# Kernel tuning notes

Measured on AMD Instinct MI355X. Metric: run time of the kernel, lower is better.

The kernel has to match this reference:

```python
import jax, jax.numpy as jnp
import numpy as np

VOCAB = 512
T = 64
D = 32
N_NODES = 4000
N_LAYERS = 5
EDGE_P = 0.03
N_BIAS = 2
SEED = 0
BATCH = 512
N_IN = T * D  # 2048 input nodes (flattened [T, d_model])


def build_graph():
    """Deterministic layered random-wired DAG.

    Node layout: [0, N_IN) inputs | [N_IN, N_IN+N_BIAS) bias(=1) |
    hidden layers | last VOCAB nodes = outputs (logits).
    An edge (u -> v) exists with prob EDGE_P for any u in an earlier
    layer than v; every non-input node gets >=1 incoming edge.
    Returns (layers, total_edges) where each layer entry is
    (src_ids, dst_local, layer_start, layer_size, w_lo, w_hi).
    """
    rng = np.random.RandomState(SEED)
    n_hidden = N_NODES - (N_IN + N_BIAS) - VOCAB
    sizes = [n_hidden // N_LAYERS + (1 if i < n_hidden % N_LAYERS else 0)
             for i in range(N_LAYERS)] + [VOCAB]
    layers = []
    start = N_IN + N_BIAS  # nodes with ids < start are valid sources
    offset = 0
    for size in sizes:
        mask = rng.random((start, size)) < EDGE_P
        empty = np.where(mask.sum(axis=0) == 0)[0]
        if empty.size:
            mask[rng.randint(0, start, empty.size), empty] = True
        src, dst = np.nonzero(mask)
        n_e = src.size
        layers.append((src.astype(np.int32), dst.astype(np.int32),
                       start, size, offset, offset + n_e))
        offset += n_e
        start += size
    return layers, offset


def setup_inputs() -> dict:
    key = jax.random.key(0)
    k1, k2, k3, k4 = jax.random.split(key, 4)
    _, n_edges = build_graph()
    return {
        "ids": jax.random.randint(k1, (BATCH, T), 0, VOCAB),
        "token_emb": jax.random.normal(k2, (VOCAB, D), dtype=jnp.float32) * 0.02,
        "pos_emb": jax.random.normal(k3, (T, D), dtype=jnp.float32) * 0.02,
        "weights": jax.random.normal(k4, (n_edges,), dtype=jnp.float32) * 0.05,
    }


def reference(ids, token_emb, pos_emb, weights):
    layers, _ = build_graph()  # static (numpy, trace-time)
    B = ids.shape[0]
    # embedding lookup + positional add, flatten to the RWNN input slab
    emb = token_emb[ids] + pos_emb[None, :, :]          # [B, T, D]
    flat = emb.reshape(B, N_IN)                          # [B, n_in]
    vals = jnp.concatenate(
        [flat, jnp.ones((B, N_BIAS), flat.dtype)], axis=1)  # [B, n_in+n_bias]
    n_layers_total = len(layers)
    for li, (src, dst, start, size, w0, w1) in enumerate(layers):
        # irregular gather over all predecessor nodes, scale, scatter-add
        msg = vals[:, src] * weights[w0:w1]              # [B, E_l]
        pre = jnp.zeros((B, size), flat.dtype).at[:, dst].add(msg)
        h = pre if li == n_layers_total - 1 else jnp.tanh(pre)
        vals = jnp.concatenate([vals, h], axis=1)
    return vals[:, -VOCAB:]                              # logits [B, V]
```

## Files before the change

### kernel.cpp

```cpp
#include <hip/hip_runtime.h>
#include <cstdint>
#include <cstdlib>
#include <cstring>
#include <vector>

#define RW_VOCAB 512
#define RW_T 64
#define RW_D 32
#define RW_NIN 2048
#define RW_NBIAS 2
#define RW_BATCH 512
#define RW_NLAYERS 6
#define RW_VBLD 4096

typedef __attribute__((ext_vector_type(8))) short short8;
typedef __attribute__((ext_vector_type(4))) float f32x4;

namespace {

struct MT19937 {
  uint32_t mt[624];
  int mti;
  void seed(uint32_t s) {
    for (int i = 0; i < 624; ++i) {
      mt[i] = s;
      s = 1812433253u * (s ^ (s >> 30)) + (uint32_t)i + 1u;
    }
    mti = 624;
  }
  inline uint32_t next() {
    if (mti >= 624) {
      for (int i = 0; i < 624; ++i) {
        uint32_t y = (mt[i] & 0x80000000u) | (mt[(i + 1) % 624] & 0x7fffffffu);
        mt[i] = mt[(i + 397) % 624] ^ (y >> 1) ^ ((y & 1u) ? 2567483615u : 0u);
      }
      mti = 0;
    }
    uint32_t y = mt[mti++];
    y ^= y >> 11;
    y ^= (y << 7) & 2636928640u;
    y ^= (y << 15) & 4022730752u;
    y ^= y >> 18;
    return y;
  }
  inline double rnd() {
    uint32_t a = next() >> 5, b = next() >> 6;
    return ((double)a * 67108864.0 + (double)b) / 9007199254740992.0;
  }
};

const int LAYER_SIZES[RW_NLAYERS] = {288, 288, 288, 287, 287, 512};
const int LAYER_START[RW_NLAYERS] = {2050, 2338, 2626, 2914, 3201, 3488};
const int LAYER_NPAD[RW_NLAYERS]  = {288, 288, 288, 288, 288, 512};
const int LAYER_NT[RW_NLAYERS]    = {9, 9, 9, 9, 9, 16};

struct GArgsH {
  int p0[RW_NLAYERS], ep[RW_NLAYERS], er[RW_NLAYERS], w0[RW_NLAYERS];
  int kpad[RW_NLAYERS];
  unsigned wofs[RW_NLAYERS];
};

struct HostGraph {
  int Epad;
  GArgsH ga;
  unsigned wdt_elems;
  uint32_t* h_pack;
};

HostGraph* build_host_graph() {
  auto* G = new HostGraph();
  MT19937 mt;
  mt.seed(0);
  std::vector<uint32_t> pack;
  pack.reserve(180000);
  int start = RW_NIN + RW_NBIAS;
  int wcum = 0;
  for (int li = 0; li < RW_NLAYERS; ++li) {
    const int size = LAYER_SIZES[li];
    G->ga.p0[li] = (int)pack.size();
    G->ga.w0[li] = wcum;
    int cnt = 0;
    for (int u = 0; u < start; ++u) {
      for (int v = 0; v < size; ++v) {
        if (mt.rnd() < 0.03) {
          pack.push_back(((uint32_t)v << 12) | (uint32_t)u);
          ++cnt;
        }
      }
    }
    G->ga.er[li] = cnt;
    wcum += cnt;
    while (pack.size() & 3u) pack.push_back(0u);
    G->ga.ep[li] = (int)pack.size() - G->ga.p0[li];
    start += size;
  }
  G->Epad = (int)pack.size();
  unsigned ofs = 0;
  for (int li = 0; li < RW_NLAYERS; ++li) {
    G->ga.kpad[li] = ((LAYER_START[li] + 63) / 64) * 64;
    G->ga.wofs[li] = ofs;
    ofs += (unsigned)LAYER_NPAD[li] * (unsigned)G->ga.kpad[li];
  }
  G->wdt_elems = ofs;
  const size_t bytes = (size_t)G->Epad * 4;
  if (hipHostMalloc((void**)&G->h_pack, bytes) != hipSuccess)
    G->h_pack = (uint32_t*)malloc(bytes);
  memcpy(G->h_pack, pack.data(), bytes);
  return G;
}

}

struct GArgs {
  int p0[RW_NLAYERS], ep[RW_NLAYERS], er[RW_NLAYERS], w0[RW_NLAYERS];
  int kpad[RW_NLAYERS];
  unsigned wofs[RW_NLAYERS];
};

__device__ __forceinline__ unsigned short f2bf(float f) {
  unsigned u = __builtin_bit_cast(unsigned, f);
  return (unsigned short)((u + 0x7fffu + ((u >> 16) & 1u)) >> 16);
}

__global__ __launch_bounds__(256) void rwnn_init(
    unsigned* __restrict__ wdt32, int nwdt32, float* __restrict__ pre,
    unsigned* __restrict__ vb32, const int* __restrict__ ids,
    const float* __restrict__ tok, const float* __restrict__ pos) {
  const int gt = blockIdx.x * 256 + threadIdx.x;
  const int gs = gridDim.x * 256;
  for (int i = gt; i < nwdt32; i += gs) wdt32[i] = 0u;
  for (int i = gt; i < RW_BATCH * 512; i += gs) pre[i] = 0.0f;
  for (int i = gt; i < RW_BATCH * (RW_VBLD / 2); i += gs) {
    const int b = i >> 11, j = i & 2047;
    const int c0 = j * 2;
    unsigned dw;
    if (c0 >= RW_NIN + RW_NBIAS) {
      dw = 0u;
    } else if (c0 == RW_NIN) {
      dw = 0x3f803f80u;
    } else {
      const int t = c0 >> 5, d = c0 & 31;
      const int id = ids[b * RW_T + t];
      const float v0 = tok[id * 32 + d] + pos[c0];
      const float v1 = tok[id * 32 + d + 1] + pos[c0 + 1];
      dw = (unsigned)f2bf(v0) | ((unsigned)f2bf(v1) << 16);
    }
    vb32[i] = dw;
  }
}

__global__ __launch_bounds__(256) void rwnn_scatter(
    const uint32_t* __restrict__ pack, const float* __restrict__ w,
    unsigned short* __restrict__ wdt, GArgs ga, int Epad) {
  const int i = blockIdx.x * 256 + threadIdx.x;
  if (i >= Epad) return;
  int l = 0;
#pragma unroll
  for (int k = 1; k < RW_NLAYERS; ++k)
    if (i >= ga.p0[k]) l = k;
  const int kk = i - ga.p0[l];
  if (kk >= ga.er[l]) return;
  const uint32_t pk = pack[i];
  const unsigned u = pk & 4095u, v = pk >> 12;
  wdt[ga.wofs[l] + (size_t)v * (unsigned)ga.kpad[l] + u] = f2bf(w[ga.w0[l] + kk]);
}

__global__ __launch_bounds__(256) void rwnn_gemm(
    const unsigned short* __restrict__ Vb, const unsigned short* __restrict__ Bt,
    float* __restrict__ pre, int kpad, int ck) {
  __shared__ unsigned short As[128][32];
  __shared__ unsigned short Bs[32][32];
  const int tid = threadIdx.x;
  const int wave = tid >> 6, lane = tid & 63;
  const int mtile = blockIdx.x, ntile = blockIdx.y;
  const int k0 = blockIdx.z * ck;
  const int k1 = min(k0 + ck, kpad);
  if (k0 >= k1) return;
  f32x4 acc[2][2] = {};
  const int sr = tid >> 2, sc = (tid & 3) * 8;
  for (int k = k0; k < k1; k += 32) {
    __syncthreads();
    {
      const float4 v0 =
          *(const float4*)(Vb + (size_t)(mtile * 128 + sr) * RW_VBLD + k + sc);
      *(float4*)(&As[sr][sc]) = v0;
      const float4 v1 = *(const float4*)(Vb +
          (size_t)(mtile * 128 + sr + 64) * RW_VBLD + k + sc);
      *(float4*)(&As[sr + 64][sc]) = v1;
    }
    if (tid < 128) {
      *(float4*)(&Bs[sr][sc]) =
          *(const float4*)(Bt + (size_t)(ntile * 32 + sr) * kpad + k + sc);
    }
    __syncthreads();
    const int lr = lane & 15, lk = (lane >> 4) * 8;
    const short8 a0 = *(const short8*)(&As[wave * 32 + lr][lk]);
    const short8 a1 = *(const short8*)(&As[wave * 32 + 16 + lr][lk]);
    const short8 b0 = *(const short8*)(&Bs[lr][lk]);
    const short8 b1 = *(const short8*)(&Bs[16 + lr][lk]);
    acc[0][0] = __builtin_amdgcn_mfma_f32_16x16x32_bf16(a0, b0, acc[0][0], 0, 0, 0);
    acc[0][1] = __builtin_amdgcn_mfma_f32_16x16x32_bf16(a0, b1, acc[0][1], 0, 0, 0);
    acc[1][0] = __builtin_amdgcn_mfma_f32_16x16x32_bf16(a1, b0, acc[1][0], 0, 0, 0);
    acc[1][1] = __builtin_amdgcn_mfma_f32_16x16x32_bf16(a1, b1, acc[1][1], 0, 0, 0);
  }
  const int lr = lane & 15, lq = lane >> 4;
#pragma unroll
  for (int ms = 0; ms < 2; ++ms)
#pragma unroll
    for (int ns = 0; ns < 2; ++ns)
#pragma unroll
      for (int r = 0; r < 4; ++r) {
        const int grow = mtile * 128 + wave * 32 + ms * 16 + lq * 4 + r;
        const int gcol = ntile * 32 + ns * 16 + lr;
        atomicAdd(pre + (size_t)grow * 512 + gcol, acc[ms][ns][r]);
      }
}

__global__ __launch_bounds__(256) void rwnn_epi(
    float* __restrict__ pre, unsigned short* __restrict__ Vb,
    float* __restrict__ out, int start, int nsize, int last) {
  const int b = blockIdx.x;
  for (int n = threadIdx.x; n < 512; n += 256) {
    const float v = pre[(size_t)b * 512 + n];
    pre[(size_t)b * 512 + n] = 0.0f;
    if (n < nsize) {
      if (last)
        out[(size_t)b * 512 + n] = v;
      else
        Vb[(size_t)b * RW_VBLD + start + n] = f2bf(tanhf(v));
    }
  }
}

__global__ __launch_bounds__(256) void rwnn_build_w(const float* __restrict__ w,
                                                    float* __restrict__ wpad,
                                                    GArgs ga, int Epad) {
  const int i = blockIdx.x * 256 + threadIdx.x;
  if (i >= Epad) return;
  int l = 0;
#pragma unroll
  for (int k = 1; k < RW_NLAYERS; ++k)
    if (i >= ga.p0[k]) l = k;
  const int kk = i - ga.p0[l];
  wpad[i] = (kk < ga.er[l]) ? w[ga.w0[l] + kk] : 0.0f;
}

__global__ __launch_bounds__(512) void rwnn_fwd_sparse(
    const int* __restrict__ ids, const float* __restrict__ tok,
    const float* __restrict__ pos, const uint32_t* __restrict__ pack,
    const float* __restrict__ wpad, float* __restrict__ out, GArgs ga) {
  __shared__ float vals[4000];
  const int b = blockIdx.x;
  const int tid = threadIdx.x;
  for (int i = tid; i < RW_NIN; i += 512) {
    const int t = i >> 5, d = i & 31;
    vals[i] = tok[(ids[b * RW_T + t] << 5) + d] + pos[i];
  }
  if (tid < RW_NBIAS) vals[RW_NIN + tid] = 1.0f;
  const int sizes[RW_NLAYERS] = {288, 288, 288, 287, 287, 512};
  int nb = RW_NIN + RW_NBIAS;
  for (int li = 0; li < RW_NLAYERS; ++li) {
    const int size = sizes[li];
    __syncthreads();
    for (int v = tid; v < size; v += 512) vals[nb + v] = 0.0f;
    __syncthreads();
    const int p0 = ga.p0[li], ng = ga.ep[li] >> 2;
    for (int g = tid; g < ng; g += 512) {
      const int e = p0 + (g << 2);
      const uint4 pk = *reinterpret_cast<const uint4*>(pack + e);
      const float4 wv = *reinterpret_cast<const float4*>(wpad + e);
      atomicAdd(&vals[nb + (pk.x >> 12)], vals[pk.x & 4095u] * wv.x);
      atomicAdd(&vals[nb + (pk.y >> 12)], vals[pk.y & 4095u] * wv.y);
      atomicAdd(&vals[nb + (pk.z >> 12)], vals[pk.z & 4095u] * wv.z);
      atomicAdd(&vals[nb + (pk.w >> 12)], vals[pk.w & 4095u] * wv.w);
    }
    __syncthreads();
    if (li == RW_NLAYERS - 1) {
      for (int v = tid; v < RW_VOCAB; v += 512) out[b * RW_VOCAB + v] = vals[nb + v];
    } else {
      for (int v = tid; v < size; v += 512) vals[nb + v] = tanhf(vals[nb + v]);
    }
    nb += size;
  }
}

extern "C" void kernel_launch(void* const* d_in, const int* in_sizes, int n_in,
                              void* d_out, int out_size, void* d_ws,
                              size_t ws_size, hipStream_t stream) {
  static HostGraph* G = build_host_graph();
  const int Epad = G->Epad;

  const int* ids = (const int*)d_in[0];
  const float* tok = (const float*)d_in[1];
  const float* pos = (const float*)d_in[2];
  const float* w = (const float*)d_in[3];
  float* out = (float*)d_out;

  GArgs ga;
  memcpy(&ga, &G->ga, sizeof(GArgs));

  char* ws = (char*)d_ws;
  const size_t packB = ((size_t)Epad * 4 + 255) & ~(size_t)255;
  const size_t wdtB = ((size_t)G->wdt_elems * 2 + 255) & ~(size_t)255;
  const size_t vbB = (size_t)RW_BATCH * RW_VBLD * 2;
  const size_t preB = (size_t)RW_BATCH * 512 * 4;
  const size_t need = packB + wdtB + vbB + preB;

  uint32_t* d_pack = (uint32_t*)ws;
  hipMemcpyAsync(d_pack, G->h_pack, (size_t)Epad * 4, hipMemcpyHostToDevice,
                 stream);

  if (ws_size < need) {
    float* d_wpad = (float*)(ws + packB);
    rwnn_build_w<<<(Epad + 255) / 256, 256, 0, stream>>>(w, d_wpad, ga, Epad);
    rwnn_fwd_sparse<<<RW_BATCH, 512, 0, stream>>>(ids, tok, pos, d_pack, d_wpad,
                                                  out, ga);
    return;
  }

  unsigned short* d_wdt = (unsigned short*)(ws + packB);
  unsigned short* d_vb = (unsigned short*)(ws + packB + wdtB);
  float* d_pre = (float*)(ws + packB + wdtB + vbB);

  rwnn_init<<<2048, 256, 0, stream>>>((unsigned*)d_wdt,
                                      (int)(G->wdt_elems / 2), d_pre,
                                      (unsigned*)d_vb, ids, tok, pos);
  rwnn_scatter<<<(Epad + 255) / 256, 256, 0, stream>>>(d_pack, w, d_wdt, ga,
                                                       Epad);
  for (int l = 0; l < RW_NLAYERS; ++l) {
    const int nt = LAYER_NT[l];
    const int SK = (l == RW_NLAYERS - 1) ? 4 : 7;
    const int kpad = ga.kpad[l];
    const int ck = (((kpad + SK - 1) / SK) + 31) & ~31;
    rwnn_gemm<<<dim3(4, nt, SK), 256, 0, stream>>>(
        d_vb, d_wdt + ga.wofs[l], d_pre, kpad, ck);
    rwnn_epi<<<RW_BATCH, 256, 0, stream>>>(d_pre, d_vb, out, LAYER_START[l],
                                           LAYER_SIZES[l],
                                           l == RW_NLAYERS - 1 ? 1 : 0);
  }
}
```

Measured before the change: 171.3 us.

## Fuse split-K reduction and tanh epilogue into GEMM via slabs and counters

The GEMM no longer atomically adds into a shared pre-activation buffer followed by a separate epilogue kernel. Each split-K block writes its partial tile to its own slab, and the last block to arrive, tracked by a per-tile atomic counter, sums the slabs and applies tanh or writes the logits. It also adds double-buffered LDS staging through global_load_lds with an XOR swizzle, and vectorizes the init kernel. This removes six epilogue launches, the float atomics and the zeroing of the pre buffer, at the cost of extra slab memory traffic and threadfence synchronization.

```diff
diff --git a/kernel.cpp b/kernel.cpp
--- a/kernel.cpp
+++ b/kernel.cpp
@@ -6,15 +6,16 @@
 
 #define RW_VOCAB 512
 #define RW_T 64
-#define RW_D 32
 #define RW_NIN 2048
 #define RW_NBIAS 2
 #define RW_BATCH 512
 #define RW_NLAYERS 6
 #define RW_VBLD 4096
+#define SLABSTRIDE (512 * 512)
 
 typedef __attribute__((ext_vector_type(8))) short short8;
 typedef __attribute__((ext_vector_type(4))) float f32x4;
+typedef uint32_t u32;
 
 namespace {
 
@@ -51,8 +52,9 @@
 
 const int LAYER_SIZES[RW_NLAYERS] = {288, 288, 288, 287, 287, 512};
 const int LAYER_START[RW_NLAYERS] = {2050, 2338, 2626, 2914, 3201, 3488};
-const int LAYER_NPAD[RW_NLAYERS]  = {288, 288, 288, 288, 288, 512};
-const int LAYER_NT[RW_NLAYERS]    = {9, 9, 9, 9, 9, 16};
+const int LAYER_NPAD[RW_NLAYERS] = {288, 288, 288, 288, 288, 512};
+const int LAYER_NT[RW_NLAYERS] = {9, 9, 9, 9, 9, 16};
+const int LAYER_SK[RW_NLAYERS] = {7, 7, 7, 7, 7, 4};
 
 struct GArgsH {
   int p0[RW_NLAYERS], ep[RW_NLAYERS], er[RW_NLAYERS], w0[RW_NLAYERS];
@@ -122,31 +124,40 @@
   return (unsigned short)((u + 0x7fffu + ((u >> 16) & 1u)) >> 16);
 }
 
+__device__ __forceinline__ void gll16(const void* g, void* l) {
+  __builtin_amdgcn_global_load_lds(
+      (const __attribute__((address_space(1))) u32*)g,
+      (__attribute__((address_space(3))) u32*)l, 16, 0, 0);
+}
+
 __global__ __launch_bounds__(256) void rwnn_init(
-    unsigned* __restrict__ wdt32, int nwdt32, float* __restrict__ pre,
-    unsigned* __restrict__ vb32, const int* __restrict__ ids,
-    const float* __restrict__ tok, const float* __restrict__ pos) {
+    uint4* __restrict__ wdt4, int n4, uint4* __restrict__ vb4,
+    const int* __restrict__ ids, const float* __restrict__ tok,
+    const float* __restrict__ pos, int* __restrict__ cnt) {
   const int gt = blockIdx.x * 256 + threadIdx.x;
   const int gs = gridDim.x * 256;
-  for (int i = gt; i < nwdt32; i += gs) wdt32[i] = 0u;
-  for (int i = gt; i < RW_BATCH * 512; i += gs) pre[i] = 0.0f;
-  for (int i = gt; i < RW_BATCH * (RW_VBLD / 2); i += gs) {
-    const int b = i >> 11, j = i & 2047;
-    const int c0 = j * 2;
-    unsigned dw;
-    if (c0 >= RW_NIN + RW_NBIAS) {
-      dw = 0u;
+  const uint4 z = {0u, 0u, 0u, 0u};
+  for (int i = gt; i < n4; i += gs) wdt4[i] = z;
+  for (int i = gt; i < RW_BATCH * (RW_VBLD / 8); i += gs) {
+    const int b = i >> 9, j = i & 511;
+    const int c0 = j * 8;
+    uint4 val = z;
+    if (c0 + 8 <= RW_NIN) {
+      const int id = ids[b * RW_T + (c0 >> 5)];
+      const float4 t0 = *(const float4*)(tok + id * 32 + (c0 & 31));
+      const float4 t1 = *(const float4*)(tok + id * 32 + (c0 & 31) + 4);
+      const float4 p0 = *(const float4*)(pos + c0);
+      const float4 p1 = *(const float4*)(pos + c0 + 4);
+      val.x = (u32)f2bf(t0.x + p0.x) | ((u32)f2bf(t0.y + p0.y) << 16);
+      val.y = (u32)f2bf(t0.z + p0.z) | ((u32)f2bf(t0.w + p0.w) << 16);
+      val.z = (u32)f2bf(t1.x + p1.x) | ((u32)f2bf(t1.y + p1.y) << 16);
+      val.w = (u32)f2bf(t1.z + p1.z) | ((u32)f2bf(t1.w + p1.w) << 16);
     } else if (c0 == RW_NIN) {
-      dw = 0x3f803f80u;
-    } else {
-      const int t = c0 >> 5, d = c0 & 31;
-      const int id = ids[b * RW_T + t];
-      const float v0 = tok[id * 32 + d] + pos[c0];
-      const float v1 = tok[id * 32 + d + 1] + pos[c0 + 1];
-      dw = (unsigned)f2bf(v0) | ((unsigned)f2bf(v1) << 16);
-    }
-    vb32[i] = dw;
-  }
+      val.x = 0x3f803f80u;
+    }
+    vb4[(size_t)b * (RW_VBLD / 8) + j] = val;
+  }
+  if (gt < RW_NLAYERS * 64) cnt[gt] = 0;
 }
 
 __global__ __launch_bounds__(256) void rwnn_scatter(
@@ -162,72 +173,112 @@
   if (kk >= ga.er[l]) return;
   const uint32_t pk = pack[i];
   const unsigned u = pk & 4095u, v = pk >> 12;
-  wdt[ga.wofs[l] + (size_t)v * (unsigned)ga.kpad[l] + u] = f2bf(w[ga.w0[l] + kk]);
-}
+  wdt[ga.wofs[l] + (size_t)v * (unsigned)ga.kpad[l] + u] =
+      f2bf(w[ga.w0[l] + kk]);
+}
+
+struct GemmP {
+  int kpad, ck, SK, nsize, vstart, last, cntofs;
+  unsigned wofs;
+};
 
 __global__ __launch_bounds__(256) void rwnn_gemm(
-    const unsigned short* __restrict__ Vb, const unsigned short* __restrict__ Bt,
-    float* __restrict__ pre, int kpad, int ck) {
-  __shared__ unsigned short As[128][32];
-  __shared__ unsigned short Bs[32][32];
+    const unsigned short* __restrict__ Vb,
+    const unsigned short* __restrict__ wdt, float* __restrict__ slab,
+    int* __restrict__ cnt, unsigned short* __restrict__ VbW,
+    float* __restrict__ out, GemmP P) {
+  __shared__ unsigned short As[2][128 * 32];
+  __shared__ unsigned short Bs[2][32 * 32];
+  __shared__ int fin;
+  const unsigned short* Bt = wdt + P.wofs;
   const int tid = threadIdx.x;
   const int wave = tid >> 6, lane = tid & 63;
-  const int mtile = blockIdx.x, ntile = blockIdx.y;
-  const int k0 = blockIdx.z * ck;
-  const int k1 = min(k0 + ck, kpad);
-  if (k0 >= k1) return;
+  const int mt = blockIdx.x, nt = blockIdx.y, sk = blockIdx.z;
+  const int k0 = sk * P.ck;
+  const int k1 = min(k0 + P.ck, P.kpad);
+  const int nit = (k1 > k0) ? ((k1 - k0 + 31) >> 5) : 0;
+
+  const int srow = tid >> 2;
+  const int schunk = tid & 3;
+
   f32x4 acc[2][2] = {};
-  const int sr = tid >> 2, sc = (tid & 3) * 8;
-  for (int k = k0; k < k1; k += 32) {
-    __syncthreads();
-    {
-      const float4 v0 =
-          *(const float4*)(Vb + (size_t)(mtile * 128 + sr) * RW_VBLD + k + sc);
-      *(float4*)(&As[sr][sc]) = v0;
-      const float4 v1 = *(const float4*)(Vb +
-          (size_t)(mtile * 128 + sr + 64) * RW_VBLD + k + sc);
-      *(float4*)(&As[sr + 64][sc]) = v1;
-    }
-    if (tid < 128) {
-      *(float4*)(&Bs[sr][sc]) =
-          *(const float4*)(Bt + (size_t)(ntile * 32 + sr) * kpad + k + sc);
-    }
-    __syncthreads();
-    const int lr = lane & 15, lk = (lane >> 4) * 8;
-    const short8 a0 = *(const short8*)(&As[wave * 32 + lr][lk]);
-    const short8 a1 = *(const short8*)(&As[wave * 32 + 16 + lr][lk]);
-    const short8 b0 = *(const short8*)(&Bs[lr][lk]);
-    const short8 b1 = *(const short8*)(&Bs[16 + lr][lk]);
+
+#define STAGE(bf, kk)                                                        \
+  do {                                                                       \
+    _Pragma("unroll") for (int j = 0; j < 2; ++j) {                          \
+      const int row_ = j * 64 + srow;                                        \
+      const int gc_ = schunk ^ (row_ & 3);                                   \
+      gll16(Vb + (size_t)(mt * 128 + row_) * RW_VBLD + (kk) + gc_ * 8,       \
+            (char*)(&As[bf][0]) + j * 4096 + wave * 1024);                   \
+    }                                                                        \
+    if (wave < 2) {                                                          \
+      const int gc_ = schunk ^ (srow & 3);                                   \
+      gll16(Bt + (size_t)(nt * 32 + srow) * P.kpad + (kk) + gc_ * 8,         \
+            (char*)(&Bs[bf][0]) + wave * 1024);                              \
+    }                                                                        \
+  } while (0)
+
+  if (nit > 0) STAGE(0, k0);
+  __syncthreads();
+
+  const int lr = lane & 15, gc4 = lane >> 4;
+  const int ra0 = wave * 32 + lr;
+  const int oa0 = ra0 * 64 + ((gc4 ^ (ra0 & 3)) << 4);
+  const int oa1 = oa0 + 16 * 64;
+  const int ob0 = lr * 64 + ((gc4 ^ (lr & 3)) << 4);
+  const int ob1 = ob0 + 16 * 64;
+
+  for (int t = 0; t < nit; ++t) {
+    const int bf = t & 1;
+    if (t + 1 < nit) STAGE(bf ^ 1, k0 + (t + 1) * 32);
+    const char* a = (const char*)&As[bf][0];
+    const char* bb = (const char*)&Bs[bf][0];
+    const short8 a0 = *(const short8*)(a + oa0);
+    const short8 a1 = *(const short8*)(a + oa1);
+    const short8 b0 = *(const short8*)(bb + ob0);
+    const short8 b1 = *(const short8*)(bb + ob1);
     acc[0][0] = __builtin_amdgcn_mfma_f32_16x16x32_bf16(a0, b0, acc[0][0], 0, 0, 0);
     acc[0][1] = __builtin_amdgcn_mfma_f32_16x16x32_bf16(a0, b1, acc[0][1], 0, 0, 0);
     acc[1][0] = __builtin_amdgcn_mfma_f32_16x16x32_bf16(a1, b0, acc[1][0], 0, 0, 0);
     acc[1][1] = __builtin_amdgcn_mfma_f32_16x16x32_bf16(a1, b1, acc[1][1], 0, 0, 0);
-  }
-  const int lr = lane & 15, lq = lane >> 4;
-#pragma unroll
-  for (int ms = 0; ms < 2; ++ms)
-#pragma unroll
-    for (int ns = 0; ns < 2; ++ns)
-#pragma unroll
-      for (int r = 0; r < 4; ++r) {
-        const int grow = mtile * 128 + wave * 32 + ms * 16 + lq * 4 + r;
-        const int gcol = ntile * 32 + ns * 16 + lr;
-        atomicAdd(pre + (size_t)grow * 512 + gcol, acc[ms][ns][r]);
-      }
-}
-
-__global__ __launch_bounds__(256) void rwnn_epi(
-    float* __restrict__ pre, unsigned short* __restrict__ Vb,
-    float* __restrict__ out, int start, int nsize, int last) {
-  const int b = blockIdx.x;
-  for (int n = threadIdx.x; n < 512; n += 256) {
-    const float v = pre[(size_t)b * 512 + n];
-    pre[(size_t)b * 512 + n] = 0.0f;
-    if (n < nsize) {
-      if (last)
-        out[(size_t)b * 512 + n] = v;
-      else
-        Vb[(size_t)b * RW_VBLD + start + n] = f2bf(tanhf(v));
+    __syncthreads();
+  }
+#undef STAGE
+
+  {
+    float* sl = slab + (size_t)sk * SLABSTRIDE;
+    const int lq = lane >> 4;
+#pragma unroll
+    for (int ms = 0; ms < 2; ++ms)
+#pragma unroll
+      for (int ns = 0; ns < 2; ++ns)
+#pragma unroll
+        for (int r = 0; r < 4; ++r) {
+          const int grow = mt * 128 + wave * 32 + ms * 16 + lq * 4 + r;
+          const int gcol = nt * 32 + ns * 16 + lr;
+          sl[(size_t)grow * 512 + gcol] = acc[ms][ns][r];
+        }
+  }
+  __syncthreads();
+  if (tid == 0) {
+    __threadfence();
+    fin = (atomicAdd(cnt + P.cntofs + mt * 16 + nt, 1) == P.SK - 1) ? 1 : 0;
+  }
+  __syncthreads();
+  if (fin) {
+    __threadfence();
+    const int c = tid & 31;
+    const int gcol = nt * 32 + c;
+    const bool wr = P.last ? true : (gcol < P.nsize);
+    for (int rr = tid >> 5; rr < 128; rr += 8) {
+      const int grow = mt * 128 + rr;
+      float s = 0.f;
+      for (int q = 0; q < P.SK; ++q)
+        s += slab[(size_t)q * SLABSTRIDE + (size_t)grow * 512 + gcol];
+      if (P.last)
+        out[(size_t)grow * 512 + gcol] = s;
+      else if (wr)
+        VbW[(size_t)grow * RW_VBLD + P.vstart + gcol] = f2bf(tanhf(s));
     }
   }
 }
@@ -276,7 +327,8 @@
     }
     __syncthreads();
     if (li == RW_NLAYERS - 1) {
-      for (int v = tid; v < RW_VOCAB; v += 512) out[b * RW_VOCAB + v] = vals[nb + v];
+      for (int v = tid; v < RW_VOCAB; v += 512)
+        out[b * RW_VOCAB + v] = vals[nb + v];
     } else {
       for (int v = tid; v < size; v += 512) vals[nb + v] = tanhf(vals[nb + v]);
     }
@@ -303,8 +355,9 @@
   const size_t packB = ((size_t)Epad * 4 + 255) & ~(size_t)255;
   const size_t wdtB = ((size_t)G->wdt_elems * 2 + 255) & ~(size_t)255;
   const size_t vbB = (size_t)RW_BATCH * RW_VBLD * 2;
-  const size_t preB = (size_t)RW_BATCH * 512 * 4;
-  const size_t need = packB + wdtB + vbB + preB;
+  const size_t slabB = (size_t)7 * SLABSTRIDE * 4;
+  const size_t cntB = RW_NLAYERS * 64 * 4;
+  const size_t need = packB + wdtB + vbB + slabB + cntB;
 
   uint32_t* d_pack = (uint32_t*)ws;
   hipMemcpyAsync(d_pack, G->h_pack, (size_t)Epad * 4, hipMemcpyHostToDevice,
@@ -313,29 +366,31 @@
   if (ws_size < need) {
     float* d_wpad = (float*)(ws + packB);
     rwnn_build_w<<<(Epad + 255) / 256, 256, 0, stream>>>(w, d_wpad, ga, Epad);
-    rwnn_fwd_sparse<<<RW_BATCH, 512, 0, stream>>>(ids, tok, pos, d_pack, d_wpad,
-                                                  out, ga);
+    rwnn_fwd_sparse<<<RW_BATCH, 512, 0, stream>>>(ids, tok, pos, d_pack,
+                                                  d_wpad, out, ga);
     return;
   }
 
   unsigned short* d_wdt = (unsigned short*)(ws + packB);
   unsigned short* d_vb = (unsigned short*)(ws + packB + wdtB);
-  float* d_pre = (float*)(ws + packB + wdtB + vbB);
-
-  rwnn_init<<<2048, 256, 0, stream>>>((unsigned*)d_wdt,
-                                      (int)(G->wdt_elems / 2), d_pre,
-                                      (unsigned*)d_vb, ids, tok, pos);
+  float* d_slab = (float*)(ws + packB + wdtB + vbB);
+  int* d_cnt = (int*)(ws + packB + wdtB + vbB + slabB);
+
+  rwnn_init<<<1024, 256, 0, stream>>>((uint4*)d_wdt, (int)(G->wdt_elems / 8),
+                                      (uint4*)d_vb, ids, tok, pos, d_cnt);
   rwnn_scatter<<<(Epad + 255) / 256, 256, 0, stream>>>(d_pack, w, d_wdt, ga,
                                                        Epad);
   for (int l = 0; l < RW_NLAYERS; ++l) {
-    const int nt = LAYER_NT[l];
-    const int SK = (l == RW_NLAYERS - 1) ? 4 : 7;
-    const int kpad = ga.kpad[l];
-    const int ck = (((kpad + SK - 1) / SK) + 31) & ~31;
-    rwnn_gemm<<<dim3(4, nt, SK), 256, 0, stream>>>(
-        d_vb, d_wdt + ga.wofs[l], d_pre, kpad, ck);
-    rwnn_epi<<<RW_BATCH, 256, 0, stream>>>(d_pre, d_vb, out, LAYER_START[l],
-                                           LAYER_SIZES[l],
-                                           l == RW_NLAYERS - 1 ? 1 : 0);
-  }
-}
+    GemmP P;
+    P.kpad = ga.kpad[l];
+    P.SK = LAYER_SK[l];
+    P.ck = ((P.kpad + P.SK - 1) / P.SK + 31) & ~31;
+    P.nsize = LAYER_SIZES[l];
+    P.vstart = LAYER_START[l];
+    P.last = (l == RW_NLAYERS - 1) ? 1 : 0;
+    P.cntofs = l * 64;
+    P.wofs = ga.wofs[l];
+    rwnn_gemm<<<dim3(4, LAYER_NT[l], P.SK), 256, 0, stream>>>(
+        d_vb, d_wdt, d_slab, d_cnt, d_vb, out, P);
+  }
+}
```

Result: slower. 382.4 us (+123.3%).

## Double K tile, swizzle LDS and prefetch next tile into registers in GEMM

Applied to the files above, without the earlier changes.

The bf16 MFMA GEMM now stages a 64-wide K slice per iteration instead of 32. It stores tiles into shared memory with an XOR swizzle to avoid bank conflicts, and loads the next K slice from global memory into registers while the current slice is being multiplied. The init kernel is also vectorised to 16-byte stores and float4 embedding loads, and launches half as many blocks. The split-K chunk is rounded to 64, so reads can run past the true K end unless kpad is padded with zeros. The early return for empty splits is also removed.

```diff
diff --git a/kernel.cpp b/kernel.cpp
--- a/kernel.cpp
+++ b/kernel.cpp
@@ -6,7 +6,6 @@
 
 #define RW_VOCAB 512
 #define RW_T 64
-#define RW_D 32
 #define RW_NIN 2048
 #define RW_NBIAS 2
 #define RW_BATCH 512
@@ -15,6 +14,7 @@
 
 typedef __attribute__((ext_vector_type(8))) short short8;
 typedef __attribute__((ext_vector_type(4))) float f32x4;
+typedef uint32_t u32;
 
 namespace {
 
@@ -51,8 +51,9 @@
 
 const int LAYER_SIZES[RW_NLAYERS] = {288, 288, 288, 287, 287, 512};
 const int LAYER_START[RW_NLAYERS] = {2050, 2338, 2626, 2914, 3201, 3488};
-const int LAYER_NPAD[RW_NLAYERS]  = {288, 288, 288, 288, 288, 512};
-const int LAYER_NT[RW_NLAYERS]    = {9, 9, 9, 9, 9, 16};
+const int LAYER_NPAD[RW_NLAYERS] = {288, 288, 288, 288, 288, 512};
+const int LAYER_NT[RW_NLAYERS] = {9, 9, 9, 9, 9, 16};
+const int LAYER_SK[RW_NLAYERS] = {7, 7, 7, 7, 7, 4};
 
 struct GArgsH {
   int p0[RW_NLAYERS], ep[RW_NLAYERS], er[RW_NLAYERS], w0[RW_NLAYERS];
@@ -123,29 +124,32 @@
 }
 
 __global__ __launch_bounds__(256) void rwnn_init(
-    unsigned* __restrict__ wdt32, int nwdt32, float* __restrict__ pre,
-    unsigned* __restrict__ vb32, const int* __restrict__ ids,
+    uint4* __restrict__ wdt4, int n4, uint4* __restrict__ pre4,
+    uint4* __restrict__ vb4, const int* __restrict__ ids,
     const float* __restrict__ tok, const float* __restrict__ pos) {
   const int gt = blockIdx.x * 256 + threadIdx.x;
   const int gs = gridDim.x * 256;
-  for (int i = gt; i < nwdt32; i += gs) wdt32[i] = 0u;
-  for (int i = gt; i < RW_BATCH * 512; i += gs) pre[i] = 0.0f;
-  for (int i = gt; i < RW_BATCH * (RW_VBLD / 2); i += gs) {
-    const int b = i >> 11, j = i & 2047;
-    const int c0 = j * 2;
-    unsigned dw;
-    if (c0 >= RW_NIN + RW_NBIAS) {
-      dw = 0u;
+  const uint4 z = {0u, 0u, 0u, 0u};
+  for (int i = gt; i < n4; i += gs) wdt4[i] = z;
+  for (int i = gt; i < RW_BATCH * 512 / 4; i += gs) pre4[i] = z;
+  for (int i = gt; i < RW_BATCH * (RW_VBLD / 8); i += gs) {
+    const int b = i >> 9, j = i & 511;
+    const int c0 = j * 8;
+    uint4 val = z;
+    if (c0 + 8 <= RW_NIN) {
+      const int id = ids[b * RW_T + (c0 >> 5)];
+      const float4 t0 = *(const float4*)(tok + id * 32 + (c0 & 31));
+      const float4 t1 = *(const float4*)(tok + id * 32 + (c0 & 31) + 4);
+      const float4 p0 = *(const float4*)(pos + c0);
+      const float4 p1 = *(const float4*)(pos + c0 + 4);
+      val.x = (u32)f2bf(t0.x + p0.x) | ((u32)f2bf(t0.y + p0.y) << 16);
+      val.y = (u32)f2bf(t0.z + p0.z) | ((u32)f2bf(t0.w + p0.w) << 16);
+      val.z = (u32)f2bf(t1.x + p1.x) | ((u32)f2bf(t1.y + p1.y) << 16);
+      val.w = (u32)f2bf(t1.z + p1.z) | ((u32)f2bf(t1.w + p1.w) << 16);
     } else if (c0 == RW_NIN) {
-      dw = 0x3f803f80u;
-    } else {
-      const int t = c0 >> 5, d = c0 & 31;
-      const int id = ids[b * RW_T + t];
-      const float v0 = tok[id * 32 + d] + pos[c0];
-      const float v1 = tok[id * 32 + d + 1] + pos[c0 + 1];
-      dw = (unsigned)f2bf(v0) | ((unsigned)f2bf(v1) << 16);
-    }
-    vb32[i] = dw;
+      val.x = 0x3f803f80u;
+    }
+    vb4[(size_t)b * (RW_VBLD / 8) + j] = val;
   }
 }
 
@@ -162,56 +166,84 @@
   if (kk >= ga.er[l]) return;
   const uint32_t pk = pack[i];
   const unsigned u = pk & 4095u, v = pk >> 12;
-  wdt[ga.wofs[l] + (size_t)v * (unsigned)ga.kpad[l] + u] = f2bf(w[ga.w0[l] + kk]);
+  wdt[ga.wofs[l] + (size_t)v * (unsigned)ga.kpad[l] + u] =
+      f2bf(w[ga.w0[l] + kk]);
 }
 
 __global__ __launch_bounds__(256) void rwnn_gemm(
-    const unsigned short* __restrict__ Vb, const unsigned short* __restrict__ Bt,
-    float* __restrict__ pre, int kpad, int ck) {
-  __shared__ unsigned short As[128][32];
-  __shared__ unsigned short Bs[32][32];
+    const unsigned short* __restrict__ Vb,
+    const unsigned short* __restrict__ Bt, float* __restrict__ pre, int kpad,
+    int ck) {
+  __shared__ unsigned short As[128 * 64];
+  __shared__ unsigned short Bs[32 * 64];
   const int tid = threadIdx.x;
   const int wave = tid >> 6, lane = tid & 63;
-  const int mtile = blockIdx.x, ntile = blockIdx.y;
-  const int k0 = blockIdx.z * ck;
+  const int mt = blockIdx.x, nt = blockIdx.y, sk = blockIdx.z;
+  const int k0 = sk * ck;
   const int k1 = min(k0 + ck, kpad);
-  if (k0 >= k1) return;
+  const int nit = (k1 - k0 + 63) >> 6;
+
+  const int arow = tid >> 3;
+  const int ach = tid & 7;
+  const int aswz = (ach ^ (arow & 7)) << 4;
+  const unsigned short* gA =
+      Vb + (size_t)(mt * 128 + arow) * RW_VBLD + ach * 8;
+  const unsigned short* gB = Bt + (size_t)(nt * 32 + arow) * kpad + ach * 8;
+  float4 pfa0, pfa1, pfa2, pfa3, pfb;
+
+#define LOADREGS(kk)                                                      \
+  do {                                                                    \
+    pfa0 = *(const float4*)(gA + (kk));                                   \
+    pfa1 = *(const float4*)(gA + (size_t)32 * RW_VBLD + (kk));            \
+    pfa2 = *(const float4*)(gA + (size_t)64 * RW_VBLD + (kk));            \
+    pfa3 = *(const float4*)(gA + (size_t)96 * RW_VBLD + (kk));            \
+    pfb = *(const float4*)(gB + (kk));                                    \
+  } while (0)
+
+  LOADREGS(k0);
+
+  const int lr = lane & 15, gc4 = lane >> 4;
   f32x4 acc[2][2] = {};
-  const int sr = tid >> 2, sc = (tid & 3) * 8;
-  for (int k = k0; k < k1; k += 32) {
-    __syncthreads();
-    {
-      const float4 v0 =
-          *(const float4*)(Vb + (size_t)(mtile * 128 + sr) * RW_VBLD + k + sc);
-      *(float4*)(&As[sr][sc]) = v0;
-      const float4 v1 = *(const float4*)(Vb +
-          (size_t)(mtile * 128 + sr + 64) * RW_VBLD + k + sc);
-      *(float4*)(&As[sr + 64][sc]) = v1;
-    }
-    if (tid < 128) {
-      *(float4*)(&Bs[sr][sc]) =
-          *(const float4*)(Bt + (size_t)(ntile * 32 + sr) * kpad + k + sc);
-    }
-    __syncthreads();
-    const int lr = lane & 15, lk = (lane >> 4) * 8;
-    const short8 a0 = *(const short8*)(&As[wave * 32 + lr][lk]);
-    const short8 a1 = *(const short8*)(&As[wave * 32 + 16 + lr][lk]);
-    const short8 b0 = *(const short8*)(&Bs[lr][lk]);
-    const short8 b1 = *(const short8*)(&Bs[16 + lr][lk]);
-    acc[0][0] = __builtin_amdgcn_mfma_f32_16x16x32_bf16(a0, b0, acc[0][0], 0, 0, 0);
-    acc[0][1] = __builtin_amdgcn_mfma_f32_16x16x32_bf16(a0, b1, acc[0][1], 0, 0, 0);
-    acc[1][0] = __builtin_amdgcn_mfma_f32_16x16x32_bf16(a1, b0, acc[1][0], 0, 0, 0);
-    acc[1][1] = __builtin_amdgcn_mfma_f32_16x16x32_bf16(a1, b1, acc[1][1], 0, 0, 0);
-  }
-  const int lr = lane & 15, lq = lane >> 4;
+
+  for (int t = 0; t < nit; ++t) {
+    __syncthreads();
+    *(float4*)((char*)As + (arow)*128 + aswz) = pfa0;
+    *(float4*)((char*)As + (32 + arow) * 128 + aswz) = pfa1;
+    *(float4*)((char*)As + (64 + arow) * 128 + aswz) = pfa2;
+    *(float4*)((char*)As + (96 + arow) * 128 + aswz) = pfa3;
+    *(float4*)((char*)Bs + arow * 128 + aswz) = pfb;
+    __syncthreads();
+    if (t + 1 < nit) LOADREGS(k0 + (t + 1) * 64);
+#pragma unroll
+    for (int kk = 0; kk < 2; ++kk) {
+      const int sa = ((kk * 4 + gc4) ^ (lr & 7)) << 4;
+      const short8 a0 =
+          *(const short8*)((char*)As + (wave * 32 + lr) * 128 + sa);
+      const short8 a1 =
+          *(const short8*)((char*)As + (wave * 32 + 16 + lr) * 128 + sa);
+      const short8 b0 = *(const short8*)((char*)Bs + lr * 128 + sa);
+      const short8 b1 = *(const short8*)((char*)Bs + (16 + lr) * 128 + sa);
+      acc[0][0] =
+          __builtin_amdgcn_mfma_f32_16x16x32_bf16(a0, b0, acc[0][0], 0, 0, 0);
+      acc[0][1] =
+          __builtin_amdgcn_mfma_f32_16x16x32_bf16(a0, b1, acc[0][1], 0, 0, 0);
+      acc[1][0] =
+          __builtin_amdgcn_mfma_f32_16x16x32_bf16(a1, b0, acc[1][0], 0, 0, 0);
+      acc[1][1] =
+          __builtin_amdgcn_mfma_f32_16x16x32_bf16(a1, b1, acc[1][1], 0, 0, 0);
+    }
+  }
+#undef LOADREGS
+
+  const int lq = lane >> 4;
 #pragma unroll
   for (int ms = 0; ms < 2; ++ms)
 #pragma unroll
     for (int ns = 0; ns < 2; ++ns)
 #pragma unroll
       for (int r = 0; r < 4; ++r) {
-        const int grow = mtile * 128 + wave * 32 + ms * 16 + lq * 4 + r;
-        const int gcol = ntile * 32 + ns * 16 + lr;
+        const int grow = mt * 128 + wave * 32 + ms * 16 + lq * 4 + r;
+        const int gcol = nt * 32 + ns * 16 + lr;
         atomicAdd(pre + (size_t)grow * 512 + gcol, acc[ms][ns][r]);
       }
 }
@@ -276,7 +308,8 @@
     }
     __syncthreads();
     if (li == RW_NLAYERS - 1) {
-      for (int v = tid; v < RW_VOCAB; v += 512) out[b * RW_VOCAB + v] = vals[nb + v];
+      for (int v = tid; v < RW_VOCAB; v += 512)
+        out[b * RW_VOCAB + v] = vals[nb + v];
     } else {
       for (int v = tid; v < size; v += 512) vals[nb + v] = tanhf(vals[nb + v]);
     }
@@ -313,8 +346,8 @@
   if (ws_size < need) {
     float* d_wpad = (float*)(ws + packB);
     rwnn_build_w<<<(Epad + 255) / 256, 256, 0, stream>>>(w, d_wpad, ga, Epad);
-    rwnn_fwd_sparse<<<RW_BATCH, 512, 0, stream>>>(ids, tok, pos, d_pack, d_wpad,
-                                                  out, ga);
+    rwnn_fwd_sparse<<<RW_BATCH, 512, 0, stream>>>(ids, tok, pos, d_pack,
+                                                  d_wpad, out, ga);
     return;
   }
 
@@ -322,17 +355,16 @@
   unsigned short* d_vb = (unsigned short*)(ws + packB + wdtB);
   float* d_pre = (float*)(ws + packB + wdtB + vbB);
 
-  rwnn_init<<<2048, 256, 0, stream>>>((unsigned*)d_wdt,
-                                      (int)(G->wdt_elems / 2), d_pre,
-                                      (unsigned*)d_vb, ids, tok, pos);
+  rwnn_init<<<1024, 256, 0, stream>>>((uint4*)d_wdt, (int)(G->wdt_elems / 8),
+                                      (uint4*)d_pre, (uint4*)d_vb, ids, tok,
+                                      pos);
   rwnn_scatter<<<(Epad + 255) / 256, 256, 0, stream>>>(d_pack, w, d_wdt, ga,
                                                        Epad);
   for (int l = 0; l < RW_NLAYERS; ++l) {
-    const int nt = LAYER_NT[l];
-    const int SK = (l == RW_NLAYERS - 1) ? 4 : 7;
+    const int SK = LAYER_SK[l];
     const int kpad = ga.kpad[l];
-    const int ck = (((kpad + SK - 1) / SK) + 31) & ~31;
-    rwnn_gemm<<<dim3(4, nt, SK), 256, 0, stream>>>(
+    const int ck = ((kpad + SK - 1) / SK + 63) & ~63;
+    rwnn_gemm<<<dim3(4, LAYER_NT[l], SK), 256, 0, stream>>>(
         d_vb, d_wdt + ga.wofs[l], d_pre, kpad, ck);
     rwnn_epi<<<RW_BATCH, 256, 0, stream>>>(d_pre, d_vb, out, LAYER_START[l],
                                            LAYER_SIZES[l],
```

After: 155.8 us. -9.0%, faster.
